# Performance work log

Hardware: AMD Instinct MI355X
Metric: run time of the kernel (lower is better)

The kernel has to match this reference:

```python
import jax, jax.numpy as jnp
import numpy as np

N_NODES = 100000
N_EDGES = 1600000
K_IND = 16          # num_indicator_weight (distance bins)
K_MLP = 16          # num_mlp_weight
DIM_HIDDEN = 64     # dim_mlp_hidden
DIST_MAX = 1.0      # distance_max
K = K_IND + K_MLP   # node feature dim / Dense output dim


def setup_inputs() -> dict:
    key = jax.random.key(0)
    ks = jax.random.split(key, 10)
    nodes = jax.random.normal(ks[0], (N_NODES, K), dtype=jnp.float32)
    distance = jax.random.uniform(ks[1], (N_EDGES,), dtype=jnp.float32) * DIST_MAX
    receivers = jnp.sort(jax.random.randint(ks[2], (N_EDGES,), 0, N_NODES, dtype=jnp.int32))
    senders = jax.random.randint(ks[3], (N_EDGES,), 0, N_NODES, dtype=jnp.int32)
    edges_padding = jnp.ones((N_EDGES,), dtype=jnp.float32)
    # MLPWeights params (Dense(1->H), Dense(H->K_MLP))
    w1 = jax.random.normal(ks[4], (1, DIM_HIDDEN), dtype=jnp.float32) / np.sqrt(1.0)
    b1 = jnp.zeros((DIM_HIDDEN,), dtype=jnp.float32)
    w2 = jax.random.normal(ks[5], (DIM_HIDDEN, K_MLP), dtype=jnp.float32) / np.sqrt(DIM_HIDDEN)
    b2 = jnp.zeros((K_MLP,), dtype=jnp.float32)
    # PowerDifference params (a=0.5, b=2)
    a = jnp.array([0.5], dtype=jnp.float32)
    b = jnp.array([2.0], dtype=jnp.float32)
    # gamma_self (no bias), gamma_gathered (with bias), both Dense(K->K)
    wg_self = jax.random.normal(ks[6], (K, K), dtype=jnp.float32) / np.sqrt(K)
    wg_gath = jax.random.normal(ks[7], (K, K), dtype=jnp.float32) / np.sqrt(K)
    bg_gath = jnp.zeros((K,), dtype=jnp.float32)
    return {"nodes": nodes, "distance": distance, "edges_padding": edges_padding,
            "receivers": receivers, "senders": senders,
            "w1": w1, "b1": b1, "w2": w2, "b2": b2,
            "a": a, "b": b, "wg_self": wg_self, "wg_gath": wg_gath, "bg_gath": bg_gath}


def _normalize_edges(edges, seg_ids, num_segments):
    sums = jax.ops.segment_sum(edges, seg_ids, num_segments=num_segments, indices_are_sorted=True)
    return edges / (sums[seg_ids] + 1e-5)


def _softmax_edges(edges, seg_ids, num_segments):
    maxs = jax.ops.segment_max(edges, seg_ids, num_segments=num_segments, indices_are_sorted=True)
    e = jnp.exp(edges - maxs[seg_ids])
    sums = jax.ops.segment_sum(e, seg_ids, num_segments=num_segments, indices_are_sorted=True)
    return e / sums[seg_ids]


def reference(nodes, distance, edges_padding, receivers, senders,
              w1, b1, w2, b2, a, b, wg_self, wg_gath, bg_gath):
    n = nodes.shape[0]
    d = distance[:, None]                                   # [E,1]
    # IndicatorWeights: bin membership via heaviside of product
    bins = jnp.linspace(0.0, DIST_MAX, K_IND + 1, dtype=nodes.dtype)
    indicator = jnp.heaviside((bins[None, :-1] - d) * (d - bins[None, 1:]), 0.0)  # [E,K_IND]
    indicator_w = _normalize_edges(indicator, receivers, n)
    # MLPWeights: Dense -> relu -> Dense, then segment softmax
    mlp = jax.nn.relu(d @ w1 + b1) @ w2 + b2                # [E,K_MLP]
    mlp_w = _softmax_edges(mlp, receivers, n)
    weights = jnp.concatenate([indicator_w, mlp_w], axis=1) * edges_padding[:, None]  # [E,K]
    # PowerDifference on gathered node pairs
    a_c = jnp.clip(a, 0.0, 1.0)
    b_c = jnp.abs(b)
    edge_pds = jnp.power(jnp.abs(a_c * nodes[receivers] - (1.0 - a_c) * nodes[senders]), b_c)  # [E,K]
    gathered = jax.ops.segment_sum(weights * edge_pds, receivers, num_segments=n, indices_are_sorted=True)  # [N,K]
    out = jax.nn.relu(nodes @ wg_self + (gathered @ wg_gath + bg_gath))
    return out
```

## Files before the change

kernel.cpp:

```cpp
#include <hip/hip_runtime.h>
#include <math.h>

#define K_TOT 32
#define K_IND 16
#define K_MLP 16
#define DHID  64


__global__ void prep_kernel(const int* __restrict__ recv, int E, int N,
                            const float* __restrict__ w1,
                            const float* __restrict__ b1,
                            const float* __restrict__ w2,
                            float* __restrict__ wsP,
                            float* __restrict__ wsN,
                            int* __restrict__ wsflag,
                            int* __restrict__ rp) {
    if (blockIdx.x == 0 && threadIdx.x < 64) {
        int t = threadIdx.x;
        if (t < K_MLP) {
            float P = 0.f, Nn = 0.f;
            for (int j = 0; j < DHID; ++j) {
                float w = w1[j];
                float v = w2[j * K_MLP + t];
                P  += fmaxf(w, 0.f) * v;
                Nn += fminf(w, 0.f) * v;
            }
            wsP[t] = P; wsN[t] = Nn;
        }
        bool nz = (b1[t] != 0.f);
        unsigned long long mask = __ballot(nz);
        if (t == 0) *wsflag = (mask == 0ull) ? 1 : 0;
    }
    int tid = blockIdx.x * blockDim.x + threadIdx.x;
    if (tid <= N) {
        int lo = 0, hi = E;
        while (lo < hi) {
            int mid = (lo + hi) >> 1;
            if (recv[mid] < tid) lo = mid + 1; else hi = mid;
        }
        rp[tid] = lo;
    }
}

__global__ __launch_bounds__(256) void graph_kernel(
        const float* __restrict__ nodes,
        const float* __restrict__ dist,
        const float* __restrict__ padv,
        const int*   __restrict__ send,
        const float* __restrict__ w1,
        const float* __restrict__ b1,
        const float* __restrict__ w2,
        const float* __restrict__ b2,
        const float* __restrict__ a_p,
        const float* __restrict__ b_p,
        const float* __restrict__ wg_self,
        const float* __restrict__ wg_gath,
        const float* __restrict__ bg,
        const float* __restrict__ wsP,
        const float* __restrict__ wsN,
        const int*   __restrict__ wsflag,
        const int*   __restrict__ rp,
        float* __restrict__ out,
        int N) {
    __shared__ __align__(16) float s_w[2048];
    __shared__ float2 s_gn[4 * 32];

    {
        int t = threadIdx.x;
        ((float4*)s_w)[t]          = ((const float4*)wg_self)[t];
        ((float4*)(s_w + 1024))[t] = ((const float4*)wg_gath)[t];
    }
    __syncthreads();

    int wave = blockIdx.x * (blockDim.x >> 6) + (threadIdx.x >> 6);
    if (wave >= N) return;
    int n    = wave;
    int lane = threadIdx.x & 63;
    int eg   = lane >> 4;
    int cc   = lane & 15;

    float a_c = fminf(fmaxf(a_p[0], 0.f), 1.f);
    float am  = 1.f - a_c;
    float bc  = fabsf(b_p[0]);

    float Pk = wsP[cc];
    float Nk = wsN[cc];

    const float* nrow = nodes + n * K_TOT;
    float nr0 = nrow[cc];
    float nr1 = nrow[cc + 16];
    float anr0 = a_c * nr0;
    float anr1 = a_c * nr1;

    int e0 = rp[n], eEnd = rp[n + 1];
    int len = eEnd - e0;

    float lo = (float)cc * 0.0625f;
    float hi = lo + 0.0625f;

    float cnt = 0.f, si = 0.f;
    float l = 0.f, acc = 0.f;
    float g_ind, g_mlp;

    bool fastf = (*wsflag != 0) && (bc == 2.0f) && (len <= 64);

    if (__builtin_amdgcn_readfirstlane((int)fastf)) {
        if (len > 0) {
            int idx = (lane < len) ? lane : (len - 1);
            int ei  = e0 + idx;
            float d_all  = dist[ei];
            int   s_all  = send[ei];
            float pe_all = padv[ei];

            float negM = -fmaxf(fabsf(Pk), fabsf(Nk));

            int nG = (len + 3) >> 2;

#define GRP_BODY(G)                                                          \
            {                                                                \
                int i = ((G) << 2) + eg;                                     \
                bool valid = i < len;                                        \
                float d  = __shfl(d_all, i);                                 \
                int   s  = __shfl(s_all, i);                                 \
                float pe = __shfl(pe_all, i);                                \
                const float* nsrow = nodes + (s * K_TOT + cc);               \
                float ns0 = nsrow[0];                                        \
                float ns1 = nsrow[16];                                       \
                float t0 = fmaf(-am, ns0, anr0);                             \
                float t1 = fmaf(-am, ns1, anr1);                             \
                float pd0 = t0 * t0;                                         \
                float pd1 = t1 * t1;                                         \
                bool inb = valid && (d > lo) && (d < hi);                    \
                cnt += inb ? 1.f : 0.f;                                      \
                si   = inb ? fmaf(pe, pd0, si) : si;                         \
                float q = (d > 0.f) ? Pk : Nk;                               \
                float p = __expf(fmaf(d, q, negM));                          \
                p = valid ? p : 0.f;                                         \
                l += p;                                                      \
                acc = fmaf(p, pe * pd1, acc);                                \
            }

            int g = 0;
            for (; g + 2 <= nG; g += 2) {
                GRP_BODY(g)
                GRP_BODY(g + 1)
            }
            if (g < nG) {
                GRP_BODY(g)
            }
#undef GRP_BODY
        }

#pragma unroll
        for (int off = 16; off <= 32; off <<= 1) {
            cnt += __shfl_xor(cnt, off);
            si  += __shfl_xor(si,  off);
            l   += __shfl_xor(l,   off);
            acc += __shfl_xor(acc, off);
        }
        g_ind = si / (cnt + 1e-5f);
        g_mlp = (l > 0.f) ? (acc / l) : 0.f;
    } else {
        float m_on = -INFINITY;
        for (int i = eg; i < len; i += 4) {
            int e = e0 + i;
            float d  = dist[e];
            int   s  = send[e];
            float pe = padv[e];
            const float* nsrow = nodes + (s * K_TOT + cc);
            float ns0 = nsrow[0];
            float ns1 = nsrow[16];
            float t0 = fabsf(fmaf(-am, ns0, anr0));
            float t1 = fabsf(fmaf(-am, ns1, anr1));
            float pd0 = powf(t0, bc);
            float pd1 = powf(t1, bc);

            bool inb = (d > lo) && (d < hi);
            cnt += inb ? 1.f : 0.f;
            si  += inb ? pe * pd0 : 0.f;

            float mlp = 0.f;
            for (int j = 0; j < DHID; ++j) {
                float h2 = fmaxf(fmaf(d, w1[j], b1[j]), 0.f);
                mlp = fmaf(h2, w2[j * K_MLP + cc], mlp);
            }
            float mn = fmaxf(m_on, mlp);
            float al = (m_on == -INFINITY) ? 0.f : __expf(m_on - mn);
            float p  = __expf(mlp - mn);
            l   = fmaf(l, al, p);
            acc = fmaf(acc, al, p * pe * pd1);
            m_on = mn;
        }
#pragma unroll
        for (int off = 16; off <= 32; off <<= 1) {
            cnt += __shfl_xor(cnt, off);
            si  += __shfl_xor(si,  off);
            float m2 = __shfl_xor(m_on, off), l2 = __shfl_xor(l, off), a2 = __shfl_xor(acc, off);
            float mn = fmaxf(m_on, m2);
            float f1 = (m_on == -INFINITY) ? 0.f : __expf(m_on - mn);
            float f2 = (m2   == -INFINITY) ? 0.f : __expf(m2 - mn);
            l   = l * f1 + l2 * f2;
            acc = acc * f1 + a2 * f2;
            m_on = mn;
        }
        g_ind = si / (cnt + 1e-5f);
        g_mlp = (l > 0.f) ? (acc / l) : 0.f;
    }

    int wv = threadIdx.x >> 6;
    float pre_g = ((lane >> 4) & 1) ? g_mlp : g_ind;
    float pre_n = ((lane >> 4) & 1) ? nr1 : nr0;
    if (lane < 32) s_gn[wv * 32 + lane] = make_float2(pre_n, pre_g);

    int h  = lane >> 5;
    int oc = lane & 31;
    const float2* gn  = s_gn + wv * 32 + h * 16;
    const float* wrow = s_w + (h * 16) * K_TOT + oc;

    float o = 0.f;
#pragma unroll
    for (int jj = 0; jj < 16; ++jj) {
        float2 v = gn[jj];
        o = fmaf(v.x, wrow[jj * K_TOT], o);
        o = fmaf(v.y, wrow[1024 + jj * K_TOT], o);
    }
    o += __shfl_xor(o, 32);
    if (h == 0) {
        out[n * K_TOT + oc] = fmaxf(o + bg[oc], 0.f);
    }
}

extern "C" void kernel_launch(void* const* d_in, const int* in_sizes, int n_in,
                              void* d_out, int out_size, void* d_ws, size_t ws_size,
                              hipStream_t stream) {
    const float* nodes   = (const float*)d_in[0];
    const float* dist    = (const float*)d_in[1];
    const float* padv    = (const float*)d_in[2];
    const int*   recv    = (const int*)d_in[3];
    const int*   send    = (const int*)d_in[4];
    const float* w1      = (const float*)d_in[5];
    const float* b1      = (const float*)d_in[6];
    const float* w2      = (const float*)d_in[7];
    const float* b2      = (const float*)d_in[8];
    const float* a_p     = (const float*)d_in[9];
    const float* b_p     = (const float*)d_in[10];
    const float* wg_self = (const float*)d_in[11];
    const float* wg_gath = (const float*)d_in[12];
    const float* bg      = (const float*)d_in[13];
    float* out = (float*)d_out;

    int N = in_sizes[0] / K_TOT;
    int E = in_sizes[1];

    float* wsf    = (float*)d_ws;
    float* wsP    = wsf;
    float* wsN    = wsf + 16;
    int*   wsflag = (int*)d_ws + 32;
    int*   rp     = (int*)d_ws + 64;

    prep_kernel<<<(N + 1 + 255) / 256, 256, 0, stream>>>(recv, E, N, w1, b1, w2,
                                                         wsP, wsN, wsflag, rp);
    graph_kernel<<<(N + 3) / 4, 256, 0, stream>>>(
        nodes, dist, padv, send, w1, b1, w2, b2, a_p, b_p,
        wg_self, wg_gath, bg, wsP, wsN, wsflag, rp, out, N);
}
```

Before: 160.0 us.

## Process four nodes per wave and interleave gamma weights in LDS

Each wavefront now loops over four consecutive receiver nodes rather than one, which amortizes block setup, the shared-memory weight load and the parameter reads across more work. The launch uses a quarter as many blocks. The self and gathered weight matrices are interleaved as float2 pairs in shared memory so the output projection needs one LDS read per pair. The fast path swaps expf and division for raw v_exp_f32 and v_rcp_f32 with pre-scaled log2e constants. Fewer waves reduce parallelism and latency hiding for the gather loads, and the fast math slightly changes rounding.

```diff
diff --git a/kernel.cpp b/kernel.cpp
--- a/kernel.cpp
+++ b/kernel.cpp
@@ -5,6 +5,15 @@
 #define K_IND 16
 #define K_MLP 16
 #define DHID  64
+#define M_NODES 4
+#define LOG2E 1.44269504088896340736f
+
+__device__ __forceinline__ float fast_rcp(float x) {
+    float r; asm("v_rcp_f32 %0, %1" : "=v"(r) : "v"(x)); return r;
+}
+__device__ __forceinline__ float fast_exp2(float x) {
+    float r; asm("v_exp_f32 %0, %1" : "=v"(r) : "v"(x)); return r;
+}
 
 
 __global__ void prep_kernel(const int* __restrict__ recv, int E, int N,
@@ -62,19 +71,26 @@
         const int*   __restrict__ rp,
         float* __restrict__ out,
         int N) {
-    __shared__ __align__(16) float s_w[2048];
-    __shared__ float2 s_gn[4 * 32];
+    __shared__ __align__(16) float2 s_wp[1024];
+    __shared__ float2 s_gn[4][32];
 
     {
         int t = threadIdx.x;
-        ((float4*)s_w)[t]          = ((const float4*)wg_self)[t];
-        ((float4*)(s_w + 1024))[t] = ((const float4*)wg_gath)[t];
+        float4 ws4 = ((const float4*)wg_self)[t];
+        float4 wg4 = ((const float4*)wg_gath)[t];
+        s_wp[t * 4 + 0] = make_float2(ws4.x, wg4.x);
+        s_wp[t * 4 + 1] = make_float2(ws4.y, wg4.y);
+        s_wp[t * 4 + 2] = make_float2(ws4.z, wg4.z);
+        s_wp[t * 4 + 3] = make_float2(ws4.w, wg4.w);
     }
     __syncthreads();
 
-    int wave = blockIdx.x * (blockDim.x >> 6) + (threadIdx.x >> 6);
-    if (wave >= N) return;
-    int n    = wave;
+    int wv   = threadIdx.x >> 6;
+    int wave = blockIdx.x * 4 + wv;
+    int n0   = wave * M_NODES;
+    if (n0 >= N) return;
+    int nEndN = n0 + M_NODES; if (nEndN > N) nEndN = N;
+
     int lane = threadIdx.x & 63;
     int eg   = lane >> 4;
     int cc   = lane & 15;
@@ -85,148 +101,156 @@
 
     float Pk = wsP[cc];
     float Nk = wsN[cc];
-
-    const float* nrow = nodes + n * K_TOT;
-    float nr0 = nrow[cc];
-    float nr1 = nrow[cc + 16];
-    float anr0 = a_c * nr0;
-    float anr1 = a_c * nr1;
-
-    int e0 = rp[n], eEnd = rp[n + 1];
-    int len = eEnd - e0;
+    float Pk2 = Pk * LOG2E;
+    float Nk2 = Nk * LOG2E;
+    float negM2 = -fmaxf(fabsf(Pk), fabsf(Nk)) * LOG2E;
 
     float lo = (float)cc * 0.0625f;
     float hi = lo + 0.0625f;
 
-    float cnt = 0.f, si = 0.f;
-    float l = 0.f, acc = 0.f;
-    float g_ind, g_mlp;
-
-    bool fastf = (*wsflag != 0) && (bc == 2.0f) && (len <= 64);
-
-    if (__builtin_amdgcn_readfirstlane((int)fastf)) {
-        if (len > 0) {
-            int idx = (lane < len) ? lane : (len - 1);
-            int ei  = e0 + idx;
-            float d_all  = dist[ei];
-            int   s_all  = send[ei];
-            float pe_all = padv[ei];
-
-            float negM = -fmaxf(fabsf(Pk), fabsf(Nk));
-
-            int nG = (len + 3) >> 2;
-
-#define GRP_BODY(G)                                                          \
-            {                                                                \
-                int i = ((G) << 2) + eg;                                     \
-                bool valid = i < len;                                        \
-                float d  = __shfl(d_all, i);                                 \
-                int   s  = __shfl(s_all, i);                                 \
-                float pe = __shfl(pe_all, i);                                \
-                const float* nsrow = nodes + (s * K_TOT + cc);               \
-                float ns0 = nsrow[0];                                        \
-                float ns1 = nsrow[16];                                       \
-                float t0 = fmaf(-am, ns0, anr0);                             \
-                float t1 = fmaf(-am, ns1, anr1);                             \
-                float pd0 = t0 * t0;                                         \
-                float pd1 = t1 * t1;                                         \
-                bool inb = valid && (d > lo) && (d < hi);                    \
-                cnt += inb ? 1.f : 0.f;                                      \
-                si   = inb ? fmaf(pe, pd0, si) : si;                         \
-                float q = (d > 0.f) ? Pk : Nk;                               \
-                float p = __expf(fmaf(d, q, negM));                          \
-                p = valid ? p : 0.f;                                         \
-                l += p;                                                      \
-                acc = fmaf(p, pe * pd1, acc);                                \
-            }
-
-            int g = 0;
-            for (; g + 2 <= nG; g += 2) {
-                GRP_BODY(g)
-                GRP_BODY(g + 1)
-            }
-            if (g < nG) {
-                GRP_BODY(g)
-            }
-#undef GRP_BODY
-        }
-
-#pragma unroll
-        for (int off = 16; off <= 32; off <<= 1) {
-            cnt += __shfl_xor(cnt, off);
-            si  += __shfl_xor(si,  off);
-            l   += __shfl_xor(l,   off);
-            acc += __shfl_xor(acc, off);
-        }
-        g_ind = si / (cnt + 1e-5f);
-        g_mlp = (l > 0.f) ? (acc / l) : 0.f;
-    } else {
-        float m_on = -INFINITY;
-        for (int i = eg; i < len; i += 4) {
-            int e = e0 + i;
-            float d  = dist[e];
-            int   s  = send[e];
-            float pe = padv[e];
-            const float* nsrow = nodes + (s * K_TOT + cc);
-            float ns0 = nsrow[0];
-            float ns1 = nsrow[16];
-            float t0 = fabsf(fmaf(-am, ns0, anr0));
-            float t1 = fabsf(fmaf(-am, ns1, anr1));
-            float pd0 = powf(t0, bc);
-            float pd1 = powf(t1, bc);
-
-            bool inb = (d > lo) && (d < hi);
-            cnt += inb ? 1.f : 0.f;
-            si  += inb ? pe * pd0 : 0.f;
-
-            float mlp = 0.f;
-            for (int j = 0; j < DHID; ++j) {
-                float h2 = fmaxf(fmaf(d, w1[j], b1[j]), 0.f);
-                mlp = fmaf(h2, w2[j * K_MLP + cc], mlp);
-            }
-            float mn = fmaxf(m_on, mlp);
-            float al = (m_on == -INFINITY) ? 0.f : __expf(m_on - mn);
-            float p  = __expf(mlp - mn);
-            l   = fmaf(l, al, p);
-            acc = fmaf(acc, al, p * pe * pd1);
-            m_on = mn;
-        }
-#pragma unroll
-        for (int off = 16; off <= 32; off <<= 1) {
-            cnt += __shfl_xor(cnt, off);
-            si  += __shfl_xor(si,  off);
-            float m2 = __shfl_xor(m_on, off), l2 = __shfl_xor(l, off), a2 = __shfl_xor(acc, off);
-            float mn = fmaxf(m_on, m2);
-            float f1 = (m_on == -INFINITY) ? 0.f : __expf(m_on - mn);
-            float f2 = (m2   == -INFINITY) ? 0.f : __expf(m2 - mn);
-            l   = l * f1 + l2 * f2;
-            acc = acc * f1 + a2 * f2;
-            m_on = mn;
-        }
-        g_ind = si / (cnt + 1e-5f);
-        g_mlp = (l > 0.f) ? (acc / l) : 0.f;
-    }
-
-    int wv = threadIdx.x >> 6;
-    float pre_g = ((lane >> 4) & 1) ? g_mlp : g_ind;
-    float pre_n = ((lane >> 4) & 1) ? nr1 : nr0;
-    if (lane < 32) s_gn[wv * 32 + lane] = make_float2(pre_n, pre_g);
+    int fastflag = (*wsflag != 0) && (bc == 2.0f);
+    float bgv = bg[lane & 31];
 
     int h  = lane >> 5;
     int oc = lane & 31;
-    const float2* gn  = s_gn + wv * 32 + h * 16;
-    const float* wrow = s_w + (h * 16) * K_TOT + oc;
-
-    float o = 0.f;
+    const float2* gnp = &s_gn[wv][h * 16];
+    const float2* wpp = &s_wp[h * 16 * 32 + oc];
+
+    int e0 = rp[n0];
+    for (int n = n0; n < nEndN; ++n) {
+        int eEnd = rp[n + 1];
+        int len  = eEnd - e0;
+
+        const float* nrow = nodes + n * K_TOT;
+        float nr0 = nrow[cc];
+        float nr1 = nrow[cc + 16];
+        float anr0 = a_c * nr0;
+        float anr1 = a_c * nr1;
+
+        float cnt = 0.f, si = 0.f;
+        float l = 0.f, acc = 0.f;
+        float g_ind, g_mlp;
+
+        if (__builtin_amdgcn_readfirstlane((int)(fastflag && (len <= 64)))) {
+            if (len > 0) {
+                int idx = (lane < len) ? lane : (len - 1);
+                int ei  = e0 + idx;
+                float d_all  = dist[ei];
+                int   s_all  = send[ei];
+                float pe_all = padv[ei];
+                d_all = (lane < len) ? d_all : 2.0f;
+
+                int nG = (len + 3) >> 2;
+
+#define GRP_BODY(G)                                                          \
+                {                                                            \
+                    int i = ((G) << 2) + eg;                                 \
+                    bool valid = i < len;                                    \
+                    float d  = __shfl(d_all, i);                             \
+                    int   s  = __shfl(s_all, i);                             \
+                    float pe = __shfl(pe_all, i);                            \
+                    const float* nsrow = nodes + (s * K_TOT + cc);           \
+                    float ns0 = nsrow[0];                                    \
+                    float ns1 = nsrow[16];                                   \
+                    float t0 = fmaf(-am, ns0, anr0);                         \
+                    float t1 = fmaf(-am, ns1, anr1);                         \
+                    float pd0 = t0 * t0;                                     \
+                    float pd1 = t1 * t1;                                     \
+                    bool inb = (d > lo) && (d < hi);                         \
+                    cnt += inb ? 1.f : 0.f;                                  \
+                    si   = inb ? fmaf(pe, pd0, si) : si;                     \
+                    float q2 = (d > 0.f) ? Pk2 : Nk2;                        \
+                    float p = fast_exp2(fmaf(d, q2, negM2));                 \
+                    p = valid ? p : 0.f;                                     \
+                    l += p;                                                  \
+                    acc = fmaf(p, pe * pd1, acc);                            \
+                }
+
+                int g = 0;
+                for (; g + 2 <= nG; g += 2) {
+                    GRP_BODY(g)
+                    GRP_BODY(g + 1)
+                }
+                if (g < nG) {
+                    GRP_BODY(g)
+                }
+#undef GRP_BODY
+            }
+
 #pragma unroll
-    for (int jj = 0; jj < 16; ++jj) {
-        float2 v = gn[jj];
-        o = fmaf(v.x, wrow[jj * K_TOT], o);
-        o = fmaf(v.y, wrow[1024 + jj * K_TOT], o);
-    }
-    o += __shfl_xor(o, 32);
-    if (h == 0) {
-        out[n * K_TOT + oc] = fmaxf(o + bg[oc], 0.f);
+            for (int off = 16; off <= 32; off <<= 1) {
+                cnt += __shfl_xor(cnt, off);
+                si  += __shfl_xor(si,  off);
+                l   += __shfl_xor(l,   off);
+                acc += __shfl_xor(acc, off);
+            }
+            g_ind = si * fast_rcp(cnt + 1e-5f);
+            g_mlp = (l > 0.f) ? (acc * fast_rcp(l)) : 0.f;
+        } else {
+            float m_on = -INFINITY;
+            for (int i = eg; i < len; i += 4) {
+                int e = e0 + i;
+                float d  = dist[e];
+                int   s  = send[e];
+                float pe = padv[e];
+                const float* nsrow = nodes + (s * K_TOT + cc);
+                float ns0 = nsrow[0];
+                float ns1 = nsrow[16];
+                float t0 = fabsf(fmaf(-am, ns0, anr0));
+                float t1 = fabsf(fmaf(-am, ns1, anr1));
+                float pd0 = powf(t0, bc);
+                float pd1 = powf(t1, bc);
+
+                bool inb = (d > lo) && (d < hi);
+                cnt += inb ? 1.f : 0.f;
+                si  += inb ? pe * pd0 : 0.f;
+
+                float mlp = 0.f;
+                for (int j = 0; j < DHID; ++j) {
+                    float h2 = fmaxf(fmaf(d, w1[j], b1[j]), 0.f);
+                    mlp = fmaf(h2, w2[j * K_MLP + cc], mlp);
+                }
+                float mn = fmaxf(m_on, mlp);
+                float al = (m_on == -INFINITY) ? 0.f : __expf(m_on - mn);
+                float p  = __expf(mlp - mn);
+                l   = fmaf(l, al, p);
+                acc = fmaf(acc, al, p * pe * pd1);
+                m_on = mn;
+            }
+#pragma unroll
+            for (int off = 16; off <= 32; off <<= 1) {
+                cnt += __shfl_xor(cnt, off);
+                si  += __shfl_xor(si,  off);
+                float m2 = __shfl_xor(m_on, off), l2 = __shfl_xor(l, off), a2 = __shfl_xor(acc, off);
+                float mn = fmaxf(m_on, m2);
+                float f1 = (m_on == -INFINITY) ? 0.f : __expf(m_on - mn);
+                float f2 = (m2   == -INFINITY) ? 0.f : __expf(m2 - mn);
+                l   = l * f1 + l2 * f2;
+                acc = acc * f1 + a2 * f2;
+                m_on = mn;
+            }
+            g_ind = si / (cnt + 1e-5f);
+            g_mlp = (l > 0.f) ? (acc / l) : 0.f;
+        }
+
+        float pre_g = ((lane >> 4) & 1) ? g_mlp : g_ind;
+        float pre_n = ((lane >> 4) & 1) ? nr1 : nr0;
+        if (lane < 32) s_gn[wv][lane] = make_float2(pre_n, pre_g);
+
+        float o = 0.f;
+#pragma unroll
+        for (int jj = 0; jj < 16; ++jj) {
+            float2 v = gnp[jj];
+            float2 w = wpp[jj * 32];
+            o = fmaf(v.x, w.x, o);
+            o = fmaf(v.y, w.y, o);
+        }
+        o += __shfl_xor(o, 32);
+        if (h == 0) {
+            out[n * K_TOT + oc] = fmaxf(o + bgv, 0.f);
+        }
+
+        e0 = eEnd;
     }
 }
 
@@ -260,7 +284,8 @@
 
     prep_kernel<<<(N + 1 + 255) / 256, 256, 0, stream>>>(recv, E, N, w1, b1, w2,
                                                          wsP, wsN, wsflag, rp);
-    graph_kernel<<<(N + 3) / 4, 256, 0, stream>>>(
+    int waves = (N + M_NODES - 1) / M_NODES;
+    graph_kernel<<<(waves + 3) / 4, 256, 0, stream>>>(
         nodes, dist, padv, send, w1, b1, w2, b2, a_p, b_p,
         wg_self, wg_gath, bg, wsP, wsN, wsflag, rp, out, N);
 }
```

After: 156.6 us. 1.02x faster.
